# Performance work log

Hardware: AMD Instinct MI355X
Metric: run time of the kernel (lower is better)

Reference implementation:

```python
import jax, jax.numpy as jnp
import numpy as np

B, D = 1024, 768


def setup_inputs() -> dict:
    key = jax.random.key(0)
    k1, k2 = jax.random.split(key)
    image_features = jax.random.normal(k1, (B, D), dtype=jnp.float32)
    # plant a few exact duplicate rows so the label-propagation path is nontrivial
    image_features = image_features.at[17].set(image_features[3])
    image_features = image_features.at[512].set(image_features[3])
    image_features = image_features.at[900].set(image_features[128])
    text_features = jax.random.normal(k2, (B, D), dtype=jnp.float32)
    logit_scale = jnp.float32(14.285714)  # exp(log(1/0.07)), standard CLIP init
    return {"image_features": image_features, "text_features": text_features, "logit_scale": logit_scale}


def reference(image_features, text_features, logit_scale):
    # logits_per_image: [B, B]
    logits = logit_scale * (image_features @ text_features.T)
    # Duplicate detection: the original O(B^2) python loop assigns to row j the
    # index of the FIRST row i (i <= j) whose features exactly equal row j.
    # eq[i, j] = rows i and j are elementwise identical
    eq = jnp.all(image_features[:, None, :] == image_features[None, :, :], axis=-1)  # [B, B] bool
    labels = jnp.argmax(eq, axis=0)  # first matching index per row (diag guarantees a hit)
    # cross-entropy with integer labels, mean over batch
    logp = jax.nn.log_softmax(logits, axis=1)
    loss = -jnp.mean(jnp.take_along_axis(logp, labels[:, None], axis=1))
    return loss
```

## Files before the change

### kernel.cpp

```cpp
#include <hip/hip_runtime.h>
#include <stdint.h>

#define BATCH 1024
#define DIM 768

typedef unsigned long long u64;
typedef __attribute__((ext_vector_type(8))) short short8;
typedef __attribute__((ext_vector_type(4))) float f32x4;

#define WS_CNT   8192
#define WS_PMAX 12288
#define WS_PSUM 28672
#define WS_LVAL 45056
#define WS_TXTB 49152

__device__ __forceinline__ unsigned short to_bf16(float x) {
    unsigned int u = __float_as_uint(x);
    return (unsigned short)((u + 0x7FFFu + ((u >> 16) & 1u)) >> 16);
}

__global__ __launch_bounds__(256) void prep_kernel(
        const float* __restrict__ img, const float* __restrict__ txt,
        u64* __restrict__ hashes, int* __restrict__ counter,
        unsigned short* __restrict__ txtB) {
    if (blockIdx.x == 0 && threadIdx.x == 0) { *counter = 0; }
    const int wave = threadIdx.x >> 6;
    const int lane = threadIdx.x & 63;

    for (int i = wave; i < 6; i += 4) {
        const int G  = blockIdx.x * 6 + i;
        const int tt = G / 24;
        const int g  = G - tt * 24;
        const int col = tt * 16 + (lane & 15);
        const int k0  = g * 32 + (lane >> 4) * 8;
        const float4 va = *(const float4*)(txt + (size_t)col * DIM + k0);
        const float4 vb = *(const float4*)(txt + (size_t)col * DIM + k0 + 4);
        short8 hv = {(short)to_bf16(va.x), (short)to_bf16(va.y),
                     (short)to_bf16(va.z), (short)to_bf16(va.w),
                     (short)to_bf16(vb.x), (short)to_bf16(vb.y),
                     (short)to_bf16(vb.z), (short)to_bf16(vb.w)};
        *(short8*)(txtB + (size_t)(g * 64 + tt) * 512 + lane * 8) = hv;
    }

    const int row = blockIdx.x * 4 + wave;
    const float4* rp = (const float4*)(img + (size_t)row * DIM);
    u64 h = 0;
#pragma unroll
    for (int c = 0; c < 3; ++c) {
        float4 v = rp[c * 64 + lane];
        int p = c * 256 + lane * 4;
        h += ((u64)__float_as_uint(v.x) + 0x9E3779B97F4A7C15ULL) * (u64)(2 * p + 1);
        h += ((u64)__float_as_uint(v.y) + 0x9E3779B97F4A7C15ULL) * (u64)(2 * p + 3);
        h += ((u64)__float_as_uint(v.z) + 0x9E3779B97F4A7C15ULL) * (u64)(2 * p + 5);
        h += ((u64)__float_as_uint(v.w) + 0x9E3779B97F4A7C15ULL) * (u64)(2 * p + 7);
    }
#pragma unroll
    for (int m = 32; m; m >>= 1) h += __shfl_xor(h, m, 64);
    if (lane == 0) hashes[row] = h;
}

__global__ __launch_bounds__(1024) void gemm_fused(
        const float* __restrict__ img, const float* __restrict__ txt,
        const float* __restrict__ scale_p, const unsigned short* __restrict__ txtB,
        const u64* __restrict__ hashes,
        float* __restrict__ pmax, float* __restrict__ psum,
        float* __restrict__ lval, int* __restrict__ counter,
        float* __restrict__ out) {
    __shared__ unsigned short Ahi[16 * DIM];
    __shared__ float logitsS[16 * 260];
    __shared__ int isLast;
    __shared__ float part[16];

    const int tid  = threadIdx.x;
    const int wave = tid >> 6;
    const int lane = tid & 63;
    const int quad = lane >> 4;
    const int l15  = lane & 15;
    const int r0    = (blockIdx.x >> 2) * 16;
    const int chunk = blockIdx.x & 3;

    {
        const float* ir = img + (size_t)(r0 + wave) * DIM;
#pragma unroll
        for (int j = 0; j < 12; ++j) {
            const int k = lane + j * 64;
            Ahi[((k >> 3) * 16 + wave) * 8 + (k & 7)] = to_bf16(ir[k]);
        }
    }
    __syncthreads();

    const int t = chunk * 16 + wave;
    const int foff = quad * 128 + l15 * 8;
    f32x4 acc = {0.f, 0.f, 0.f, 0.f};
#pragma unroll
    for (int kk = 0; kk < 24; ++kk) {
        const short8 a = *(const short8*)&Ahi[kk * 512 + foff];
        const short8 b = *(const short8*)(txtB + (size_t)(kk * 64 + t) * 512 + foff);
        acc = __builtin_amdgcn_mfma_f32_16x16x32_bf16(a, b, acc, 0, 0, 0);
    }

    const float scale = scale_p[0];
#pragma unroll
    for (int r = 0; r < 4; ++r)
        logitsS[(quad * 4 + r) * 260 + wave * 16 + l15] = scale * acc[r];
    __syncthreads();

    {
        const float4 f = *(const float4*)&logitsS[wave * 260 + lane * 4];
        float mx = fmaxf(fmaxf(f.x, f.y), fmaxf(f.z, f.w));
#pragma unroll
        for (int s = 32; s; s >>= 1) mx = fmaxf(mx, __shfl_xor(mx, s, 64));
        float sum = __expf(f.x - mx) + __expf(f.y - mx) +
                    __expf(f.z - mx) + __expf(f.w - mx);
#pragma unroll
        for (int s = 32; s; s >>= 1) sum += __shfl_xor(sum, s, 64);
        if (lane == 0) {
            atomicExch(&pmax[(r0 + wave) * 4 + chunk], mx);
            atomicExch(&psum[(r0 + wave) * 4 + chunk], sum);
        }
    }

    if (wave < 4) {
        const int j = r0 + chunk * 4 + wave;
        const u64 hj = hashes[j];
        int lo = -1;
        int label = j;
        for (;;) {
            int cand = BATCH;
#pragma unroll
            for (int it = 0; it < 16; ++it) {
                const int i = lane + it * 64;
                const u64 h = hashes[i];
                if (i < j && i > lo && h == hj) cand = min(cand, i);
            }
#pragma unroll
            for (int s = 32; s; s >>= 1) cand = min(cand, __shfl_xor(cand, s, 64));
            if (cand >= j) break;
            const float4* rpm = (const float4*)(img + (size_t)cand * DIM);
            const float4* rpj = (const float4*)(img + (size_t)j * DIM);
            bool eq = true;
#pragma unroll
            for (int c = 0; c < 3; ++c) {
                float4 vm = rpm[c * 64 + lane];
                float4 vj = rpj[c * 64 + lane];
                eq = eq && (vm.x == vj.x) && (vm.y == vj.y) &&
                     (vm.z == vj.z) && (vm.w == vj.w);
            }
            if (__all(eq)) { label = cand; break; }
            lo = cand;
        }

        const float4* aj = (const float4*)(img + (size_t)j * DIM);
        const float4* bl = (const float4*)(txt + (size_t)label * DIM);
        float s = 0.0f;
#pragma unroll
        for (int c = 0; c < 3; ++c) {
            const float4 va = aj[c * 64 + lane];
            const float4 vb = bl[c * 64 + lane];
            s += va.x * vb.x + va.y * vb.y + va.z * vb.z + va.w * vb.w;
        }
#pragma unroll
        for (int m = 32; m; m >>= 1) s += __shfl_xor(s, m, 64);
        if (lane == 0) atomicExch(&lval[j], scale * s);
    }

    __syncthreads();
    if (tid == 0) {
        __threadfence();
        isLast = (atomicAdd(counter, 1) == (int)gridDim.x - 1) ? 1 : 0;
    }
    __syncthreads();
    if (!isLast) return;
    __threadfence();

    {
        const float4 m4 = *(const float4*)&pmax[tid * 4];
        const float4 s4 = *(const float4*)&psum[tid * 4];
        const float lv = lval[tid];
        const float gmax = fmaxf(fmaxf(m4.x, m4.y), fmaxf(m4.z, m4.w));
        const float ss = s4.x * __expf(m4.x - gmax) + s4.y * __expf(m4.y - gmax)
                       + s4.z * __expf(m4.z - gmax) + s4.w * __expf(m4.w - gmax);
        float loss = gmax + __logf(ss) - lv;
#pragma unroll
        for (int m = 32; m; m >>= 1) loss += __shfl_xor(loss, m, 64);
        if (lane == 0) part[wave] = loss;
        __syncthreads();
        if (tid == 0) {
            float tot = 0.0f;
#pragma unroll
            for (int w = 0; w < 16; ++w) tot += part[w];
            out[0] = tot * (1.0f / BATCH);
        }
    }
}

extern "C" void kernel_launch(void* const* d_in, const int* in_sizes, int n_in,
                              void* d_out, int out_size, void* d_ws, size_t ws_size,
                              hipStream_t stream) {
    const float* img   = (const float*)d_in[0];
    const float* txt   = (const float*)d_in[1];
    const float* scale = (const float*)d_in[2];
    float* out = (float*)d_out;
    char* ws = (char*)d_ws;

    u64*   hashes  = (u64*)ws;
    int*   counter = (int*)(ws + WS_CNT);
    float* pmax    = (float*)(ws + WS_PMAX);
    float* psum    = (float*)(ws + WS_PSUM);
    float* lval    = (float*)(ws + WS_LVAL);
    unsigned short* txtB = (unsigned short*)(ws + WS_TXTB);

    prep_kernel<<<256, 256, 0, stream>>>(img, txt, hashes, counter, txtB);
    gemm_fused<<<256, 1024, 0, stream>>>(img, txt, scale, txtB, hashes,
                                         pmax, psum, lval, counter, out);
}
```

Baseline: 79.38 us.

## Merge prep and GEMM kernels using a grid-wide spin barrier

Folds the text bf16 conversion and row hashing into the main kernel, using spare waves of each 1024-thread block, and replaces the kernel boundary with a global atomic counter barrier that spins. The counters are reset with a memset instead of inside the prep kernel. This removes one kernel launch and its gap, and overlaps the A-tile staging with prep work. In exchange it adds a memset launch, and it relies on all 256 blocks being resident at once, which could deadlock if they are not.

```diff
diff --git a/kernel.cpp b/kernel.cpp
--- a/kernel.cpp
+++ b/kernel.cpp
@@ -8,7 +8,8 @@
 typedef __attribute__((ext_vector_type(8))) short short8;
 typedef __attribute__((ext_vector_type(4))) float f32x4;
 
-#define WS_CNT   8192
+#define WS_DONE  8192
+#define WS_TAIL  8196
 #define WS_PMAX 12288
 #define WS_PSUM 28672
 #define WS_LVAL 45056
@@ -19,20 +20,41 @@
     return (unsigned short)((u + 0x7FFFu + ((u >> 16) & 1u)) >> 16);
 }
 
-__global__ __launch_bounds__(256) void prep_kernel(
+__global__ __launch_bounds__(1024) void fused_kernel(
         const float* __restrict__ img, const float* __restrict__ txt,
-        u64* __restrict__ hashes, int* __restrict__ counter,
-        unsigned short* __restrict__ txtB) {
-    if (blockIdx.x == 0 && threadIdx.x == 0) { *counter = 0; }
-    const int wave = threadIdx.x >> 6;
-    const int lane = threadIdx.x & 63;
-
-    for (int i = wave; i < 6; i += 4) {
-        const int G  = blockIdx.x * 6 + i;
+        const float* __restrict__ scale_p, u64* __restrict__ hashes,
+        unsigned short* __restrict__ txtB,
+        float* __restrict__ pmax, float* __restrict__ psum,
+        float* __restrict__ lval, int* __restrict__ done,
+        int* __restrict__ tailcnt, float* __restrict__ out) {
+    __shared__ unsigned short Ahi[16 * DIM];
+    __shared__ float logitsS[16 * 260];
+    __shared__ int isLast;
+    __shared__ float part[16];
+
+    const int tid  = threadIdx.x;
+    const int wave = tid >> 6;
+    const int lane = tid & 63;
+    const int quad = lane >> 4;
+    const int l15  = lane & 15;
+    const int r0    = (blockIdx.x >> 2) * 16;
+    const int chunk = blockIdx.x & 3;
+
+    {
+        const float* ir = img + (size_t)(r0 + wave) * DIM;
+#pragma unroll
+        for (int j = 0; j < 12; ++j) {
+            const int k = lane + j * 64;
+            Ahi[((k >> 3) * 16 + wave) * 8 + (k & 7)] = to_bf16(ir[k]);
+        }
+    }
+
+    if (wave < 6) {
+        const int G  = blockIdx.x * 6 + wave;
         const int tt = G / 24;
         const int g  = G - tt * 24;
-        const int col = tt * 16 + (lane & 15);
-        const int k0  = g * 32 + (lane >> 4) * 8;
+        const int col = tt * 16 + l15;
+        const int k0  = g * 32 + quad * 8;
         const float4 va = *(const float4*)(txt + (size_t)col * DIM + k0);
         const float4 vb = *(const float4*)(txt + (size_t)col * DIM + k0 + 4);
         short8 hv = {(short)to_bf16(va.x), (short)to_bf16(va.y),
@@ -42,52 +64,34 @@
         *(short8*)(txtB + (size_t)(g * 64 + tt) * 512 + lane * 8) = hv;
     }
 
-    const int row = blockIdx.x * 4 + wave;
-    const float4* rp = (const float4*)(img + (size_t)row * DIM);
-    u64 h = 0;
-#pragma unroll
-    for (int c = 0; c < 3; ++c) {
-        float4 v = rp[c * 64 + lane];
-        int p = c * 256 + lane * 4;
-        h += ((u64)__float_as_uint(v.x) + 0x9E3779B97F4A7C15ULL) * (u64)(2 * p + 1);
-        h += ((u64)__float_as_uint(v.y) + 0x9E3779B97F4A7C15ULL) * (u64)(2 * p + 3);
-        h += ((u64)__float_as_uint(v.z) + 0x9E3779B97F4A7C15ULL) * (u64)(2 * p + 5);
-        h += ((u64)__float_as_uint(v.w) + 0x9E3779B97F4A7C15ULL) * (u64)(2 * p + 7);
-    }
-#pragma unroll
-    for (int m = 32; m; m >>= 1) h += __shfl_xor(h, m, 64);
-    if (lane == 0) hashes[row] = h;
-}
-
-__global__ __launch_bounds__(1024) void gemm_fused(
-        const float* __restrict__ img, const float* __restrict__ txt,
-        const float* __restrict__ scale_p, const unsigned short* __restrict__ txtB,
-        const u64* __restrict__ hashes,
-        float* __restrict__ pmax, float* __restrict__ psum,
-        float* __restrict__ lval, int* __restrict__ counter,
-        float* __restrict__ out) {
-    __shared__ unsigned short Ahi[16 * DIM];
-    __shared__ float logitsS[16 * 260];
-    __shared__ int isLast;
-    __shared__ float part[16];
-
-    const int tid  = threadIdx.x;
-    const int wave = tid >> 6;
-    const int lane = tid & 63;
-    const int quad = lane >> 4;
-    const int l15  = lane & 15;
-    const int r0    = (blockIdx.x >> 2) * 16;
-    const int chunk = blockIdx.x & 3;
-
-    {
-        const float* ir = img + (size_t)(r0 + wave) * DIM;
-#pragma unroll
-        for (int j = 0; j < 12; ++j) {
-            const int k = lane + j * 64;
-            Ahi[((k >> 3) * 16 + wave) * 8 + (k & 7)] = to_bf16(ir[k]);
-        }
-    }
-    __syncthreads();
+    if (wave >= 6 && wave < 10) {
+        const int row = blockIdx.x * 4 + (wave - 6);
+        const float4* rp = (const float4*)(img + (size_t)row * DIM);
+        u64 h = 0;
+#pragma unroll
+        for (int c = 0; c < 3; ++c) {
+            float4 v = rp[c * 64 + lane];
+            int p = c * 256 + lane * 4;
+            h += ((u64)__float_as_uint(v.x) + 0x9E3779B97F4A7C15ULL) * (u64)(2 * p + 1);
+            h += ((u64)__float_as_uint(v.y) + 0x9E3779B97F4A7C15ULL) * (u64)(2 * p + 3);
+            h += ((u64)__float_as_uint(v.z) + 0x9E3779B97F4A7C15ULL) * (u64)(2 * p + 5);
+            h += ((u64)__float_as_uint(v.w) + 0x9E3779B97F4A7C15ULL) * (u64)(2 * p + 7);
+        }
+#pragma unroll
+        for (int m = 32; m; m >>= 1) h += __shfl_xor(h, m, 64);
+        if (lane == 0) hashes[row] = h;
+    }
+
+    __threadfence();
+    __syncthreads();
+    if (tid == 0) {
+        __hip_atomic_fetch_add(done, 1, __ATOMIC_RELEASE, __HIP_MEMORY_SCOPE_AGENT);
+        while (__hip_atomic_load(done, __ATOMIC_RELAXED, __HIP_MEMORY_SCOPE_AGENT)
+               < (int)gridDim.x)
+            __builtin_amdgcn_s_sleep(8);
+    }
+    __syncthreads();
+    __threadfence();
 
     const int t = chunk * 16 + wave;
     const int foff = quad * 128 + l15 * 8;
@@ -167,7 +171,7 @@
     __syncthreads();
     if (tid == 0) {
         __threadfence();
-        isLast = (atomicAdd(counter, 1) == (int)gridDim.x - 1) ? 1 : 0;
+        isLast = (atomicAdd(tailcnt, 1) == (int)gridDim.x - 1) ? 1 : 0;
     }
     __syncthreads();
     if (!isLast) return;
@@ -204,13 +208,14 @@
     char* ws = (char*)d_ws;
 
     u64*   hashes  = (u64*)ws;
-    int*   counter = (int*)(ws + WS_CNT);
+    int*   done    = (int*)(ws + WS_DONE);
+    int*   tailcnt = (int*)(ws + WS_TAIL);
     float* pmax    = (float*)(ws + WS_PMAX);
     float* psum    = (float*)(ws + WS_PSUM);
     float* lval    = (float*)(ws + WS_LVAL);
     unsigned short* txtB = (unsigned short*)(ws + WS_TXTB);
 
-    prep_kernel<<<256, 256, 0, stream>>>(img, txt, hashes, counter, txtB);
-    gemm_fused<<<256, 1024, 0, stream>>>(img, txt, scale, txtB, hashes,
-                                         pmax, psum, lval, counter, out);
+    hipMemsetAsync(ws + WS_DONE, 0, 8, stream);
+    fused_kernel<<<256, 1024, 0, stream>>>(img, txt, scale, hashes, txtB,
+                                           pmax, psum, lval, done, tailcnt, out);
 }
```

Measured after the change: 227.5 us. 2.87x slower.

## Fuse prep into GEMM kernel: convert text to bf16 inline, prefilter duplicates by first two floats

Applied to the files above, without the earlier changes.

Drops the separate prep kernel. The GEMM now reads fp32 text rows directly and converts them to bf16 inside the MFMA loop, with no pre-packed bf16 copy. Duplicate candidates are prefiltered by comparing each row's first two floats instead of a precomputed row hash, and the tail counter is reset with a memset. This removes one kernel launch and the write and re-read of the bf16 text buffer and hashes. In exchange it adds redundant fp32 loads and conversions of the text matrix across blocks, a weaker prefilter that may trigger more full-row compares, and a memset node.

```diff
diff --git a/kernel.cpp b/kernel.cpp
--- a/kernel.cpp
+++ b/kernel.cpp
@@ -8,63 +8,21 @@
 typedef __attribute__((ext_vector_type(8))) short short8;
 typedef __attribute__((ext_vector_type(4))) float f32x4;
 
-#define WS_CNT   8192
-#define WS_PMAX 12288
-#define WS_PSUM 28672
-#define WS_LVAL 45056
-#define WS_TXTB 49152
+#define WS_TAIL     0
+#define WS_PMAX  4096
+#define WS_PSUM 20480
+#define WS_LVAL 36864
 
 __device__ __forceinline__ unsigned short to_bf16(float x) {
     unsigned int u = __float_as_uint(x);
     return (unsigned short)((u + 0x7FFFu + ((u >> 16) & 1u)) >> 16);
 }
 
-__global__ __launch_bounds__(256) void prep_kernel(
+__global__ __launch_bounds__(1024) void fused_kernel(
         const float* __restrict__ img, const float* __restrict__ txt,
-        u64* __restrict__ hashes, int* __restrict__ counter,
-        unsigned short* __restrict__ txtB) {
-    if (blockIdx.x == 0 && threadIdx.x == 0) { *counter = 0; }
-    const int wave = threadIdx.x >> 6;
-    const int lane = threadIdx.x & 63;
-
-    for (int i = wave; i < 6; i += 4) {
-        const int G  = blockIdx.x * 6 + i;
-        const int tt = G / 24;
-        const int g  = G - tt * 24;
-        const int col = tt * 16 + (lane & 15);
-        const int k0  = g * 32 + (lane >> 4) * 8;
-        const float4 va = *(const float4*)(txt + (size_t)col * DIM + k0);
-        const float4 vb = *(const float4*)(txt + (size_t)col * DIM + k0 + 4);
-        short8 hv = {(short)to_bf16(va.x), (short)to_bf16(va.y),
-                     (short)to_bf16(va.z), (short)to_bf16(va.w),
-                     (short)to_bf16(vb.x), (short)to_bf16(vb.y),
-                     (short)to_bf16(vb.z), (short)to_bf16(vb.w)};
-        *(short8*)(txtB + (size_t)(g * 64 + tt) * 512 + lane * 8) = hv;
-    }
-
-    const int row = blockIdx.x * 4 + wave;
-    const float4* rp = (const float4*)(img + (size_t)row * DIM);
-    u64 h = 0;
-#pragma unroll
-    for (int c = 0; c < 3; ++c) {
-        float4 v = rp[c * 64 + lane];
-        int p = c * 256 + lane * 4;
-        h += ((u64)__float_as_uint(v.x) + 0x9E3779B97F4A7C15ULL) * (u64)(2 * p + 1);
-        h += ((u64)__float_as_uint(v.y) + 0x9E3779B97F4A7C15ULL) * (u64)(2 * p + 3);
-        h += ((u64)__float_as_uint(v.z) + 0x9E3779B97F4A7C15ULL) * (u64)(2 * p + 5);
-        h += ((u64)__float_as_uint(v.w) + 0x9E3779B97F4A7C15ULL) * (u64)(2 * p + 7);
-    }
-#pragma unroll
-    for (int m = 32; m; m >>= 1) h += __shfl_xor(h, m, 64);
-    if (lane == 0) hashes[row] = h;
-}
-
-__global__ __launch_bounds__(1024) void gemm_fused(
-        const float* __restrict__ img, const float* __restrict__ txt,
-        const float* __restrict__ scale_p, const unsigned short* __restrict__ txtB,
-        const u64* __restrict__ hashes,
+        const float* __restrict__ scale_p,
         float* __restrict__ pmax, float* __restrict__ psum,
-        float* __restrict__ lval, int* __restrict__ counter,
+        float* __restrict__ lval, int* __restrict__ tailcnt,
         float* __restrict__ out) {
     __shared__ unsigned short Ahi[16 * DIM];
     __shared__ float logitsS[16 * 260];
@@ -91,11 +49,17 @@
 
     const int t = chunk * 16 + wave;
     const int foff = quad * 128 + l15 * 8;
+    const float* tp = txt + (size_t)(t * 16 + l15) * DIM + quad * 8;
     f32x4 acc = {0.f, 0.f, 0.f, 0.f};
 #pragma unroll
     for (int kk = 0; kk < 24; ++kk) {
         const short8 a = *(const short8*)&Ahi[kk * 512 + foff];
-        const short8 b = *(const short8*)(txtB + (size_t)(kk * 64 + t) * 512 + foff);
+        const float4 va = *(const float4*)(tp + kk * 32);
+        const float4 vb = *(const float4*)(tp + kk * 32 + 4);
+        const short8 b = {(short)to_bf16(va.x), (short)to_bf16(va.y),
+                          (short)to_bf16(va.z), (short)to_bf16(va.w),
+                          (short)to_bf16(vb.x), (short)to_bf16(vb.y),
+                          (short)to_bf16(vb.z), (short)to_bf16(vb.w)};
         acc = __builtin_amdgcn_mfma_f32_16x16x32_bf16(a, b, acc, 0, 0, 0);
     }
 
@@ -122,7 +86,7 @@
 
     if (wave < 4) {
         const int j = r0 + chunk * 4 + wave;
-        const u64 hj = hashes[j];
+        const float2 sj = *(const float2*)(img + (size_t)j * DIM);
         int lo = -1;
         int label = j;
         for (;;) {
@@ -130,8 +94,9 @@
 #pragma unroll
             for (int it = 0; it < 16; ++it) {
                 const int i = lane + it * 64;
-                const u64 h = hashes[i];
-                if (i < j && i > lo && h == hj) cand = min(cand, i);
+                const float2 si = *(const float2*)(img + (size_t)i * DIM);
+                if (i < j && i > lo && si.x == sj.x && si.y == sj.y)
+                    cand = min(cand, i);
             }
 #pragma unroll
             for (int s = 32; s; s >>= 1) cand = min(cand, __shfl_xor(cand, s, 64));
@@ -167,7 +132,7 @@
     __syncthreads();
     if (tid == 0) {
         __threadfence();
-        isLast = (atomicAdd(counter, 1) == (int)gridDim.x - 1) ? 1 : 0;
+        isLast = (atomicAdd(tailcnt, 1) == (int)gridDim.x - 1) ? 1 : 0;
     }
     __syncthreads();
     if (!isLast) return;
@@ -203,14 +168,12 @@
     float* out = (float*)d_out;
     char* ws = (char*)d_ws;
 
-    u64*   hashes  = (u64*)ws;
-    int*   counter = (int*)(ws + WS_CNT);
+    int*   tailcnt = (int*)(ws + WS_TAIL);
     float* pmax    = (float*)(ws + WS_PMAX);
     float* psum    = (float*)(ws + WS_PSUM);
     float* lval    = (float*)(ws + WS_LVAL);
-    unsigned short* txtB = (unsigned short*)(ws + WS_TXTB);
 
-    prep_kernel<<<256, 256, 0, stream>>>(img, txt, hashes, counter, txtB);
-    gemm_fused<<<256, 1024, 0, stream>>>(img, txt, scale, txtB, hashes,
-                                         pmax, psum, lval, counter, out);
+    hipMemsetAsync(ws + WS_TAIL, 0, 4, stream);
+    fused_kernel<<<256, 1024, 0, stream>>>(img, txt, scale,
+                                           pmax, psum, lval, tailcnt, out);
 }
```

Result: slower. 100.5 us (+26.6%).
